# Kernel tuning notes

Measured on AMD Instinct MI355X. Metric: run time of the kernel, lower is better.

## Reference

```python
import jax, jax.numpy as jnp
import numpy as np

N_NODES = 50000
N_EDGES = 600000
D = 128
R = 8


def setup_inputs() -> dict:
    key = jax.random.key(0)
    ks = jax.random.split(key, 10)
    return {
        "node_ids": jnp.arange(N_NODES, dtype=jnp.int32),
        "src": jax.random.randint(ks[0], (N_EDGES,), 0, N_NODES, dtype=jnp.int32),
        "dst": jax.random.randint(ks[1], (N_EDGES,), 0, N_NODES, dtype=jnp.int32),
        "etype": jax.random.randint(ks[2], (N_EDGES,), 0, R, dtype=jnp.int32),
        "emb": jax.random.normal(ks[3], (N_NODES, D), dtype=jnp.float32) * 0.02,
        "W1": jax.random.normal(ks[4], (R, D, D), dtype=jnp.float32) * 0.05,
        "Wself1": jax.random.normal(ks[5], (D, D), dtype=jnp.float32) * 0.05,
        "b1": jnp.zeros((D,), dtype=jnp.float32),
        "W2": jax.random.normal(ks[6], (R, D, D), dtype=jnp.float32) * 0.05,
        "Wself2": jax.random.normal(ks[7], (D, D), dtype=jnp.float32) * 0.05,
        "b2": jnp.zeros((D,), dtype=jnp.float32),
    }


def rgcn_layer(h, W, Wself, b, src, dst, etype, n_nodes):
    # relation-wise transform of all node features: [R, N, d_out]
    hr = jnp.einsum('nd,rdo->rno', h, W)
    # per-edge gather of (relation, src) -> message, then scatter-sum to dst
    msgs = hr[etype, src]                                   # [E, d_out]
    agg = jax.ops.segment_sum(msgs, dst, num_segments=n_nodes)
    # self-loop + bias (activation=None, feat_drop=0)
    return agg + h @ Wself + b


def reference(node_ids, src, dst, etype, emb, W1, Wself1, b1, W2, Wself2, b2):
    h0 = emb[node_ids]                                      # embedding lookup over all nodes
    h1 = rgcn_layer(h0, W1, Wself1, b1, src, dst, etype, emb.shape[0])
    h2 = rgcn_layer(h1, W2, Wself2, b2, src, dst, etype, emb.shape[0])
    return h2
```

## Files before the change

kernel.cpp:

```cpp
#include <hip/hip_runtime.h>
#include <hip/hip_bf16.h>

#define NN 50000
#define NE 600000
#define DD 128
#define NR 8
#define NCHUNK ((NN + 255) / 256)

typedef __attribute__((ext_vector_type(8))) short bf16x8;
typedef __attribute__((ext_vector_type(4))) float f32x4;

__device__ __forceinline__ unsigned short f2bf(float f) {
  __hip_bfloat16 h = __float2bfloat16(f);
  return *reinterpret_cast<unsigned short*>(&h);
}
__device__ __forceinline__ unsigned pk2(float lo, float hi) {
  return (unsigned)f2bf(lo) | ((unsigned)f2bf(hi) << 16);
}
__device__ __forceinline__ float bflo(unsigned u) { return __uint_as_float(u << 16); }
__device__ __forceinline__ float bfhi(unsigned u) { return __uint_as_float(u & 0xffff0000u); }

__global__ __launch_bounds__(128) void convw_kernel(
    const float* __restrict__ W1, const float* __restrict__ Ws1,
    const float* __restrict__ W2, const float* __restrict__ Ws2,
    unsigned short* __restrict__ WT)
{
  const int m = blockIdx.y, o = blockIdx.x, d = threadIdx.x;
  const float* src;
  if (m < 8)       src = W1 + (size_t)m * DD * DD;
  else if (m == 8) src = Ws1;
  else if (m < 17) src = W2 + (size_t)(m - 9) * DD * DD;
  else             src = Ws2;
  WT[(size_t)m * DD * DD + o * DD + d] = f2bf(src[(size_t)d * DD + o]);
}

__global__ __launch_bounds__(256) void convh_kernel(
    const float* __restrict__ emb, const int* __restrict__ ids,
    unsigned short* __restrict__ h)
{
  const int gid = blockIdx.x * 256 + threadIdx.x;
  if (gid >= NN * 16) return;
  const int row = gid >> 4;
  const int off = (gid & 15) * 8;
  const int srcRow = ids[row];
  const float* src = emb + (size_t)srcRow * DD + off;
  const float4 a = *reinterpret_cast<const float4*>(src);
  const float4 b = *reinterpret_cast<const float4*>(src + 4);
  uint4 u;
  u.x = pk2(a.x, a.y); u.y = pk2(a.z, a.w);
  u.z = pk2(b.x, b.y); u.w = pk2(b.z, b.w);
  *reinterpret_cast<uint4*>(h + (size_t)row * DD + off) = u;
}

__global__ __launch_bounds__(256) void hist_kernel(
    const int* __restrict__ dst, int* __restrict__ deg)
{
  const int e = blockIdx.x * 256 + threadIdx.x;
  if (e < NE) atomicAdd(&deg[dst[e]], 1);
}

__global__ __launch_bounds__(256) void bsum_kernel(
    const int* __restrict__ deg, int* __restrict__ bsum)
{
  __shared__ int tmp[256];
  const int t = threadIdx.x;
  const int i = blockIdx.x * 256 + t;
  tmp[t] = (i < NN) ? deg[i] : 0;
  __syncthreads();
#pragma unroll
  for (int off = 128; off > 0; off >>= 1) {
    if (t < off) tmp[t] += tmp[t + off];
    __syncthreads();
  }
  if (t == 0) bsum[blockIdx.x] = tmp[0];
}

__global__ __launch_bounds__(256) void bscan_kernel(
    const int* __restrict__ bsum, int* __restrict__ bbase)
{
  __shared__ int tmp[256];
  const int t = threadIdx.x;
  const int v = (t < NCHUNK) ? bsum[t] : 0;
  tmp[t] = v;
  __syncthreads();
#pragma unroll
  for (int off = 1; off < 256; off <<= 1) {
    const int x = (t >= off) ? tmp[t - off] : 0;
    __syncthreads();
    tmp[t] += x;
    __syncthreads();
  }
  if (t < NCHUNK) bbase[t] = tmp[t] - v;
}

__global__ __launch_bounds__(256) void expand_kernel(
    int* deg, const int* __restrict__ bbase, int* __restrict__ offsets)
{
  __shared__ int tmp[256];
  const int t = threadIdx.x;
  const int i = blockIdx.x * 256 + t;
  const int v = (i < NN) ? deg[i] : 0;
  tmp[t] = v;
  __syncthreads();
#pragma unroll
  for (int off = 1; off < 256; off <<= 1) {
    const int x = (t >= off) ? tmp[t - off] : 0;
    __syncthreads();
    tmp[t] += x;
    __syncthreads();
  }
  const int base = bbase[blockIdx.x];
  const int excl = base + tmp[t] - v;
  if (i < NN) {
    offsets[i] = excl;
    deg[i] = excl;
    if (i == NN - 1) offsets[NN] = base + tmp[t];
  }
}

__global__ __launch_bounds__(256) void fill_kernel(
    const int* __restrict__ src, const int* __restrict__ dst,
    const int* __restrict__ et, int* __restrict__ cursor,
    int* __restrict__ eidx)
{
  const int e = blockIdx.x * 256 + threadIdx.x;
  if (e < NE) {
    const int pos = atomicAdd(&cursor[dst[e]], 1);
    eidx[pos] = (src[e] << 3) | et[e];
  }
}

__global__ __launch_bounds__(256) void agg_kernel(
    const unsigned short* __restrict__ h,
    const int* __restrict__ offsets, const int* __restrict__ eidx,
    unsigned short* __restrict__ s)
{
  const int node = blockIdx.x * 4 + (threadIdx.x >> 6);
  const int lane = threadIdx.x & 63;
  if (node >= NN) return;
  const int beg = offsets[node];
  const int end = offsets[node + 1];

  float ax[NR], ay[NR];
#pragma unroll
  for (int r = 0; r < NR; ++r) { ax[r] = 0.f; ay[r] = 0.f; }

  int e = beg;
  for (; e + 1 < end; e += 2) {
    const int v0 = eidx[e], v1 = eidx[e + 1];
    const unsigned u0 = *reinterpret_cast<const unsigned*>(h + (size_t)(v0 >> 3) * DD + lane * 2);
    const unsigned u1 = *reinterpret_cast<const unsigned*>(h + (size_t)(v1 >> 3) * DD + lane * 2);
    const int e0 = v0 & 7, e1 = v1 & 7;
    const float x0 = bflo(u0), y0 = bfhi(u0), x1 = bflo(u1), y1 = bfhi(u1);
#pragma unroll
    for (int r = 0; r < NR; ++r) {
      ax[r] += ((e0 == r) ? x0 : 0.f) + ((e1 == r) ? x1 : 0.f);
      ay[r] += ((e0 == r) ? y0 : 0.f) + ((e1 == r) ? y1 : 0.f);
    }
  }
  if (e < end) {
    const int v0 = eidx[e];
    const unsigned u0 = *reinterpret_cast<const unsigned*>(h + (size_t)(v0 >> 3) * DD + lane * 2);
    const int e0 = v0 & 7;
    const float x0 = bflo(u0), y0 = bfhi(u0);
#pragma unroll
    for (int r = 0; r < NR; ++r) {
      ax[r] += (e0 == r) ? x0 : 0.f;
      ay[r] += (e0 == r) ? y0 : 0.f;
    }
  }

  unsigned short* srow = s + (size_t)node * (NR * DD) + lane * 2;
#pragma unroll
  for (int r = 0; r < NR; ++r)
    *reinterpret_cast<unsigned*>(srow + r * DD) = pk2(ax[r], ay[r]);
}

template<int OUTF32>
__global__ __launch_bounds__(256) void gemm_kernel(
    const unsigned short* __restrict__ hbuf,
    const unsigned short* __restrict__ s,
    const unsigned short* __restrict__ WTl,
    const float* __restrict__ bias,
    void* __restrict__ out)
{
  __shared__ __align__(16) char ldsW[2][DD * DD * 2];

  const int tid = threadIdx.x;
  const int rowBase = blockIdx.x * 128;
  const int lane = tid & 63;
  const int w = tid >> 6;
  const int c = lane & 15;
  const int g = lane >> 4;
  int nn[2], nld[2];
#pragma unroll
  for (int u = 0; u < 2; ++u) {
    nn[u] = rowBase + w * 32 + u * 16 + c;
    nld[u] = (nn[u] < NN) ? nn[u] : (NN - 1);
  }

  int srcOff[8];
#pragma unroll
  for (int j = 0; j < 8; ++j) {
    const int dstB = (tid + j * 256) * 16;
    const int srcB = dstB ^ (((dstB >> 8) & 7) << 4);
    srcOff[j] = srcB >> 1;
  }

  uint4 wreg[8];
#pragma unroll
  for (int j = 0; j < 8; ++j)
    wreg[j] = *reinterpret_cast<const uint4*>(WTl + srcOff[j]);
#pragma unroll
  for (int j = 0; j < 8; ++j)
    *reinterpret_cast<uint4*>(ldsW[0] + (tid + j * 256) * 16) = wreg[j];

  bf16x8 sfA[2][4], sfB[2][4];
#pragma unroll
  for (int u = 0; u < 2; ++u) {
    const unsigned short* p0 = s + (size_t)nld[u] * (NR * DD);
#pragma unroll
    for (int ks = 0; ks < 4; ++ks)
      sfA[u][ks] = *reinterpret_cast<const bf16x8*>(p0 + ks * 32 + g * 8);
  }

  f32x4 acc[2][8];
#pragma unroll
  for (int u = 0; u < 2; ++u)
#pragma unroll
    for (int t = 0; t < 8; ++t) acc[u][t] = (f32x4){0.f, 0.f, 0.f, 0.f};

#define GSTEP(R, CUR, NXT)                                                            \
  {                                                                                   \
    __syncthreads();                                                                  \
    const char* buf = ldsW[(R) & 1];                                                  \
    if ((R) < NR) {                                                                   \
      const unsigned short* wnext = WTl + (size_t)((R) + 1) * DD * DD;                \
      _Pragma("unroll")                                                               \
      for (int j = 0; j < 8; ++j)                                                     \
        wreg[j] = *reinterpret_cast<const uint4*>(wnext + srcOff[j]);                 \
      _Pragma("unroll")                                                               \
      for (int u = 0; u < 2; ++u) {                                                   \
        const unsigned short* pn = ((R) + 1 < NR)                                     \
            ? s + (size_t)nld[u] * (NR * DD) + ((R) + 1) * DD                         \
            : hbuf + (size_t)nld[u] * DD;                                             \
        _Pragma("unroll")                                                             \
        for (int ks = 0; ks < 4; ++ks)                                                \
          NXT[u][ks] = *reinterpret_cast<const bf16x8*>(pn + ks * 32 + g * 8);        \
      }                                                                               \
    }                                                                                 \
    _Pragma("unroll")                                                                 \
    for (int ks = 0; ks < 4; ++ks) {                                                  \
      _Pragma("unroll")                                                               \
      for (int t = 0; t < 8; ++t) {                                                   \
        const int addr = (((t * 16 + c) << 8) + (ks << 6) + (g << 4)) ^ ((c & 7) << 4); \
        bf16x8 a = *reinterpret_cast<const bf16x8*>(buf + addr);                      \
        acc[0][t] = __builtin_amdgcn_mfma_f32_16x16x32_bf16(a, CUR[0][ks], acc[0][t], 0, 0, 0); \
        acc[1][t] = __builtin_amdgcn_mfma_f32_16x16x32_bf16(a, CUR[1][ks], acc[1][t], 0, 0, 0); \
      }                                                                               \
    }                                                                                 \
    if ((R) < NR) {                                                                   \
      char* nbuf = ldsW[((R) & 1) ^ 1];                                               \
      _Pragma("unroll")                                                               \
      for (int j = 0; j < 8; ++j)                                                     \
        *reinterpret_cast<uint4*>(nbuf + (tid + j * 256) * 16) = wreg[j];             \
    }                                                                                 \
  }

  GSTEP(0, sfA, sfB) GSTEP(1, sfB, sfA) GSTEP(2, sfA, sfB) GSTEP(3, sfB, sfA)
  GSTEP(4, sfA, sfB) GSTEP(5, sfB, sfA) GSTEP(6, sfA, sfB) GSTEP(7, sfB, sfA)
  GSTEP(8, sfA, sfB)
#undef GSTEP

#pragma unroll
  for (int u = 0; u < 2; ++u) {
    const int n = nn[u];
    if (n >= NN) continue;
    if (OUTF32) {
      float* dst = (float*)out + (size_t)n * DD;
#pragma unroll
      for (int t = 0; t < 8; ++t) {
        const int o0 = t * 16 + g * 4;
        const float4 bv = *reinterpret_cast<const float4*>(bias + o0);
        float4 o;
        o.x = acc[u][t][0] + bv.x; o.y = acc[u][t][1] + bv.y;
        o.z = acc[u][t][2] + bv.z; o.w = acc[u][t][3] + bv.w;
        *reinterpret_cast<float4*>(dst + o0) = o;
      }
    } else {
      unsigned short* dst = (unsigned short*)out + (size_t)n * DD;
#pragma unroll
      for (int t = 0; t < 8; ++t) {
        const int o0 = t * 16 + g * 4;
        const float4 bv = *reinterpret_cast<const float4*>(bias + o0);
        uint2 q;
        q.x = pk2(acc[u][t][0] + bv.x, acc[u][t][1] + bv.y);
        q.y = pk2(acc[u][t][2] + bv.z, acc[u][t][3] + bv.w);
        *reinterpret_cast<uint2*>(dst + o0) = q;
      }
    }
  }
}

extern "C" void kernel_launch(void* const* d_in, const int* in_sizes, int n_in,
                              void* d_out, int out_size, void* d_ws, size_t ws_size,
                              hipStream_t stream) {
  const int*   node_ids = (const int*)d_in[0];
  const int*   src   = (const int*)d_in[1];
  const int*   dst   = (const int*)d_in[2];
  const int*   etype = (const int*)d_in[3];
  const float* emb   = (const float*)d_in[4];
  const float* W1    = (const float*)d_in[5];
  const float* Ws1   = (const float*)d_in[6];
  const float* b1    = (const float*)d_in[7];
  const float* W2    = (const float*)d_in[8];
  const float* Ws2   = (const float*)d_in[9];
  const float* b2    = (const float*)d_in[10];

  char* p = (char*)d_ws;
  unsigned short* s    = (unsigned short*)p;  p += (size_t)NN * NR * DD * 2;
  unsigned short* hbuf = (unsigned short*)p;  p += (size_t)NN * DD * 2;
  unsigned short* WT   = (unsigned short*)p;  p += (size_t)18 * DD * DD * 2;
  int* offsets         = (int*)p;             p += (size_t)(NN + 1) * 4;
  int* deg             = (int*)p;             p += (size_t)NN * 4;
  int* eidx            = (int*)p;             p += (size_t)NE * 4;
  int* bsum            = (int*)p;             p += 256 * 4;
  int* bbase           = (int*)p;

  const int eb = (NE + 255) / 256;
  const int tb = (NN + 127) / 128;
  const int ab = (NN + 3) / 4;

  convw_kernel<<<dim3(DD, 18), 128, 0, stream>>>(W1, Ws1, W2, Ws2, WT);
  convh_kernel<<<(NN * 16) / 256, 256, 0, stream>>>(emb, node_ids, hbuf);
  hipMemsetAsync(deg, 0, (size_t)NN * 4, stream);
  hist_kernel<<<eb, 256, 0, stream>>>(dst, deg);
  bsum_kernel<<<NCHUNK, 256, 0, stream>>>(deg, bsum);
  bscan_kernel<<<1, 256, 0, stream>>>(bsum, bbase);
  expand_kernel<<<NCHUNK, 256, 0, stream>>>(deg, bbase, offsets);
  fill_kernel<<<eb, 256, 0, stream>>>(src, dst, etype, deg, eidx);

  agg_kernel<<<ab, 256, 0, stream>>>(hbuf, offsets, eidx, s);
  gemm_kernel<0><<<tb, 256, 0, stream>>>(hbuf, s, WT, b1, hbuf);
  agg_kernel<<<ab, 256, 0, stream>>>(hbuf, offsets, eidx, s);
  gemm_kernel<1><<<tb, 256, 0, stream>>>(hbuf, s, WT + (size_t)9 * DD * DD, b2, (float*)d_out);
}
```

Before: 259.4 us.

## Bucket edges by (dst, relation) CSR to drop per-edge relation select

The CSR build now keys edges by dst*NR+etype, so each node's edges arrive grouped by relation and eidx holds only the source id. The aggregation kernel loops over the eight relation segments and accumulates into a single pair of scalars, replacing eight-way predicated adds per edge. The cost is a histogram, scan and offset array eight times larger, a multi-element-per-thread block scan, and more per-segment loop overhead with odd-count tails.

```diff
diff --git a/kernel.cpp b/kernel.cpp
--- a/kernel.cpp
+++ b/kernel.cpp
@@ -5,7 +5,9 @@
 #define NE 600000
 #define DD 128
 #define NR 8
-#define NCHUNK ((NN + 255) / 256)
+#define NB (NN * NR)
+#define NCHUNK8 ((NB + 255) / 256)
+#define PERT ((NCHUNK8 + 255) / 256)
 
 typedef __attribute__((ext_vector_type(8))) short bf16x8;
 typedef __attribute__((ext_vector_type(4))) float f32x4;
@@ -53,10 +55,11 @@
 }
 
 __global__ __launch_bounds__(256) void hist_kernel(
-    const int* __restrict__ dst, int* __restrict__ deg)
+    const int* __restrict__ dst, const int* __restrict__ et,
+    int* __restrict__ deg)
 {
   const int e = blockIdx.x * 256 + threadIdx.x;
-  if (e < NE) atomicAdd(&deg[dst[e]], 1);
+  if (e < NE) atomicAdd(&deg[dst[e] * NR + et[e]], 1);
 }
 
 __global__ __launch_bounds__(256) void bsum_kernel(
@@ -65,7 +68,7 @@
   __shared__ int tmp[256];
   const int t = threadIdx.x;
   const int i = blockIdx.x * 256 + t;
-  tmp[t] = (i < NN) ? deg[i] : 0;
+  tmp[t] = (i < NB) ? deg[i] : 0;
   __syncthreads();
 #pragma unroll
   for (int off = 128; off > 0; off >>= 1) {
@@ -80,8 +83,11 @@
 {
   __shared__ int tmp[256];
   const int t = threadIdx.x;
-  const int v = (t < NCHUNK) ? bsum[t] : 0;
-  tmp[t] = v;
+  const int b = t * PERT;
+  const int e = min(b + PERT, NCHUNK8);
+  int s = 0;
+  for (int i = b; i < e; ++i) s += bsum[i];
+  tmp[t] = s;
   __syncthreads();
 #pragma unroll
   for (int off = 1; off < 256; off <<= 1) {
@@ -90,7 +96,12 @@
     tmp[t] += x;
     __syncthreads();
   }
-  if (t < NCHUNK) bbase[t] = tmp[t] - v;
+  int run = tmp[t] - s;
+  for (int i = b; i < e; ++i) {
+    const int v = bsum[i];
+    bbase[i] = run;
+    run += v;
+  }
 }
 
 __global__ __launch_bounds__(256) void expand_kernel(
@@ -99,7 +110,7 @@
   __shared__ int tmp[256];
   const int t = threadIdx.x;
   const int i = blockIdx.x * 256 + t;
-  const int v = (i < NN) ? deg[i] : 0;
+  const int v = (i < NB) ? deg[i] : 0;
   tmp[t] = v;
   __syncthreads();
 #pragma unroll
@@ -111,10 +122,10 @@
   }
   const int base = bbase[blockIdx.x];
   const int excl = base + tmp[t] - v;
-  if (i < NN) {
+  if (i < NB) {
     offsets[i] = excl;
     deg[i] = excl;
-    if (i == NN - 1) offsets[NN] = base + tmp[t];
+    if (i == NB - 1) offsets[NB] = base + tmp[t];
   }
 }
 
@@ -125,55 +136,43 @@
 {
   const int e = blockIdx.x * 256 + threadIdx.x;
   if (e < NE) {
-    const int pos = atomicAdd(&cursor[dst[e]], 1);
-    eidx[pos] = (src[e] << 3) | et[e];
+    const int pos = atomicAdd(&cursor[dst[e] * NR + et[e]], 1);
+    eidx[pos] = src[e];
   }
 }
 
 __global__ __launch_bounds__(256) void agg_kernel(
     const unsigned short* __restrict__ h,
-    const int* __restrict__ offsets, const int* __restrict__ eidx,
+    const int* __restrict__ off8, const int* __restrict__ eidx,
     unsigned short* __restrict__ s)
 {
   const int node = blockIdx.x * 4 + (threadIdx.x >> 6);
   const int lane = threadIdx.x & 63;
   if (node >= NN) return;
-  const int beg = offsets[node];
-  const int end = offsets[node + 1];
-
-  float ax[NR], ay[NR];
-#pragma unroll
-  for (int r = 0; r < NR; ++r) { ax[r] = 0.f; ay[r] = 0.f; }
-
-  int e = beg;
-  for (; e + 1 < end; e += 2) {
-    const int v0 = eidx[e], v1 = eidx[e + 1];
-    const unsigned u0 = *reinterpret_cast<const unsigned*>(h + (size_t)(v0 >> 3) * DD + lane * 2);
-    const unsigned u1 = *reinterpret_cast<const unsigned*>(h + (size_t)(v1 >> 3) * DD + lane * 2);
-    const int e0 = v0 & 7, e1 = v1 & 7;
-    const float x0 = bflo(u0), y0 = bfhi(u0), x1 = bflo(u1), y1 = bfhi(u1);
-#pragma unroll
-    for (int r = 0; r < NR; ++r) {
-      ax[r] += ((e0 == r) ? x0 : 0.f) + ((e1 == r) ? x1 : 0.f);
-      ay[r] += ((e0 == r) ? y0 : 0.f) + ((e1 == r) ? y1 : 0.f);
+  const unsigned short* hp = h + lane * 2;
+  unsigned short* srow = s + (size_t)node * (NR * DD) + lane * 2;
+
+  int b = off8[node * NR];
+#pragma unroll
+  for (int r = 0; r < NR; ++r) {
+    const int e2 = off8[node * NR + r + 1];
+    float ax = 0.f, ay = 0.f;
+    int e = b;
+    for (; e + 1 < e2; e += 2) {
+      const int s0 = eidx[e], s1 = eidx[e + 1];
+      const unsigned u0 = *reinterpret_cast<const unsigned*>(hp + (size_t)s0 * DD);
+      const unsigned u1 = *reinterpret_cast<const unsigned*>(hp + (size_t)s1 * DD);
+      ax += bflo(u0) + bflo(u1);
+      ay += bfhi(u0) + bfhi(u1);
     }
-  }
-  if (e < end) {
-    const int v0 = eidx[e];
-    const unsigned u0 = *reinterpret_cast<const unsigned*>(h + (size_t)(v0 >> 3) * DD + lane * 2);
-    const int e0 = v0 & 7;
-    const float x0 = bflo(u0), y0 = bfhi(u0);
-#pragma unroll
-    for (int r = 0; r < NR; ++r) {
-      ax[r] += (e0 == r) ? x0 : 0.f;
-      ay[r] += (e0 == r) ? y0 : 0.f;
+    if (e < e2) {
+      const unsigned u0 = *reinterpret_cast<const unsigned*>(hp + (size_t)eidx[e] * DD);
+      ax += bflo(u0);
+      ay += bfhi(u0);
     }
-  }
-
-  unsigned short* srow = s + (size_t)node * (NR * DD) + lane * 2;
-#pragma unroll
-  for (int r = 0; r < NR; ++r)
-    *reinterpret_cast<unsigned*>(srow + r * DD) = pk2(ax[r], ay[r]);
+    *reinterpret_cast<unsigned*>(srow + r * DD) = pk2(ax, ay);
+    b = e2;
+  }
 }
 
 template<int OUTF32>
@@ -321,10 +320,10 @@
   unsigned short* s    = (unsigned short*)p;  p += (size_t)NN * NR * DD * 2;
   unsigned short* hbuf = (unsigned short*)p;  p += (size_t)NN * DD * 2;
   unsigned short* WT   = (unsigned short*)p;  p += (size_t)18 * DD * DD * 2;
-  int* offsets         = (int*)p;             p += (size_t)(NN + 1) * 4;
-  int* deg             = (int*)p;             p += (size_t)NN * 4;
+  int* off8            = (int*)p;             p += (size_t)(NB + 1) * 4;
+  int* deg8            = (int*)p;             p += (size_t)NB * 4;
   int* eidx            = (int*)p;             p += (size_t)NE * 4;
-  int* bsum            = (int*)p;             p += 256 * 4;
+  int* bsum            = (int*)p;             p += (size_t)NCHUNK8 * 4;
   int* bbase           = (int*)p;
 
   const int eb = (NE + 255) / 256;
@@ -333,15 +332,15 @@
 
   convw_kernel<<<dim3(DD, 18), 128, 0, stream>>>(W1, Ws1, W2, Ws2, WT);
   convh_kernel<<<(NN * 16) / 256, 256, 0, stream>>>(emb, node_ids, hbuf);
-  hipMemsetAsync(deg, 0, (size_t)NN * 4, stream);
-  hist_kernel<<<eb, 256, 0, stream>>>(dst, deg);
-  bsum_kernel<<<NCHUNK, 256, 0, stream>>>(deg, bsum);
+  hipMemsetAsync(deg8, 0, (size_t)NB * 4, stream);
+  hist_kernel<<<eb, 256, 0, stream>>>(dst, etype, deg8);
+  bsum_kernel<<<NCHUNK8, 256, 0, stream>>>(deg8, bsum);
   bscan_kernel<<<1, 256, 0, stream>>>(bsum, bbase);
-  expand_kernel<<<NCHUNK, 256, 0, stream>>>(deg, bbase, offsets);
-  fill_kernel<<<eb, 256, 0, stream>>>(src, dst, etype, deg, eidx);
-
-  agg_kernel<<<ab, 256, 0, stream>>>(hbuf, offsets, eidx, s);
+  expand_kernel<<<NCHUNK8, 256, 0, stream>>>(deg8, bbase, off8);
+  fill_kernel<<<eb, 256, 0, stream>>>(src, dst, etype, deg8, eidx);
+
+  agg_kernel<<<ab, 256, 0, stream>>>(hbuf, off8, eidx, s);
   gemm_kernel<0><<<tb, 256, 0, stream>>>(hbuf, s, WT, b1, hbuf);
-  agg_kernel<<<ab, 256, 0, stream>>>(hbuf, offsets, eidx, s);
+  agg_kernel<<<ab, 256, 0, stream>>>(hbuf, off8, eidx, s);
   gemm_kernel<1><<<tb, 256, 0, stream>>>(hbuf, s, WT + (size_t)9 * DD * DD, b2, (float*)d_out);
 }
```

After: 273.5 us. +5.4%, slower.
